# Kernel tuning notes

Measured on AMD Instinct MI355X. Metric: run time of the kernel, lower is better.

Reference implementation:

```python
import jax, jax.numpy as jnp
import numpy as np
from jax import lax

DT = 0.1


def setup_inputs() -> dict:
    key = jax.random.key(0)
    k1, k2, k3, k4 = jax.random.split(key, 4)
    Bsz, L, D, N, O = 32, 2048, 256, 64, 256
    x = jax.random.normal(k1, (Bsz, L, D), dtype=jnp.float32)
    # Shift A by 3*I so Re(eig(A)) > 0 -> bilinear-discretized A_tilde is stable
    A = jax.random.uniform(k2, (N, N), dtype=jnp.float32) + 3.0 * jnp.eye(N, dtype=jnp.float32)
    B = jax.random.uniform(k3, (N, D), dtype=jnp.float32)
    C = jax.random.uniform(k4, (O, N), dtype=jnp.float32)
    return {"x": x, "A": A, "B": B, "C": C}


def _s4_forward(x, A, B, C):
    N = A.shape[0]
    I = jnp.eye(N, dtype=A.dtype)
    # Bilinear discretization (as written in the torch source)
    tmp_inv = jnp.linalg.inv(I + A * (DT / 2))
    A_tilde = tmp_inv @ (I - A * (DT / 2))          # [N, N]
    B_tilde = (tmp_inv @ B) * DT                    # [N, D]

    L = x.shape[1]

    # K[i] = C @ A_tilde^i @ B_tilde; carry M = A_tilde^i @ B_tilde
    def step(M, _):
        return A_tilde @ M, C @ M                    # emit [O, D]

    _, K = lax.scan(step, B_tilde, None, length=L)   # K: [L, O, D]

    n = 2 * L - 1  # length after torch's F.pad(x, (0,0,0,L-1))
    x_fft = jnp.fft.rfft(x, n=n, axis=1)             # [B, F, D] complex
    K_fft = jnp.fft.rfft(K, n=n, axis=0)             # [F, O, D] complex
    y_fft = jnp.einsum('bfi,foi->bfo', x_fft, K_fft)
    y = jnp.fft.irfft(y_fft, n=n, axis=1)[:, :L]     # [B, L, O]
    return y


def reference(x, A, B, C):
    return _s4_forward(x, A, B, C)
```

## Files before the change

### kernel.cpp

```cpp
#include <hip/hip_runtime.h>

#define B_SZ   32
#define LEN    2048
#define DIM    256
#define NST    64
#define OUTD   256
#define CHUNK  64
#define NCHUNK (LEN / CHUNK)
#define ROWS   (B_SZ * LEN)

#define OFF_AT   0
#define OFF_A64  4096
#define OFF_MT   8192
#define OFF_S    12288
#define OFF_INST 77824
#define OFF_U    143360
#define OFF_H    4337664
#define OFF_V    OFF_H
#define WS_FLOATS (OFF_H + ROWS * 64)

__global__ __launch_bounds__(256) void k_fused0(const float* __restrict__ A,
                                                const float* __restrict__ Bm,
                                                const float* __restrict__ x,
                                                float* __restrict__ ws) {
  __shared__ __align__(16) float sh[9088];
  const int t = threadIdx.x;

  if (blockIdx.x == 0) {
    float* Pa  = sh;
    float* Pb  = sh + 4352;
    float* rbM = sh + 8704;
    float* rbI = sh + 8832;
    float* cb  = sh + 8960;

    const int tc = t & 63;
    const int tr = t >> 6;
    float M[16], Iv[16];
    for (int i = 0; i < 16; ++i) {
      int r = 16 * tr + i;
      M[i] = 0.05f * A[r * 64 + tc] + (r == tc ? 1.0f : 0.0f);
      Iv[i] = (r == tc) ? 1.0f : 0.0f;
    }
    if (tr == 0) { rbM[tc] = M[0]; rbI[tc] = Iv[0]; }
    if (tc == 0)
      for (int i = 0; i < 16; ++i) cb[16 * tr + i] = M[i];
    __syncthreads();

#pragma unroll
    for (int k = 0; k < 64; ++k) {
      const int cur = (k & 1) * 64, nxt = ((k + 1) & 1) * 64;
      float rinv = 1.0f / rbM[cur + k];
      float rM = rbM[cur + tc] * rinv;
      float rI = rbI[cur + tc] * rinv;
#pragma unroll
      for (int i = 0; i < 16; ++i) {
        int r = 16 * tr + i;
        if (r == k) { M[i] = rM; Iv[i] = rI; }
        else {
          float f = cb[cur + r];
          M[i] = fmaf(-f, rM, M[i]);
          Iv[i] = fmaf(-f, rI, Iv[i]);
        }
      }
      if (k < 63) {
        if (tr == ((k + 1) >> 4)) {
          rbM[nxt + tc] = M[(k + 1) & 15];
          rbI[nxt + tc] = Iv[(k + 1) & 15];
        }
        if (tc == k + 1)
          for (int i = 0; i < 16; ++i) cb[nxt + 16 * tr + i] = M[i];
      }
      __syncthreads();
    }

    for (int i = 0; i < 16; ++i) {
      int r = 16 * tr + i;
      ws[OFF_AT + r * 64 + tc] = 2.0f * Iv[i] - (r == tc ? 1.0f : 0.0f);
      Pa[r * 65 + tc] = Iv[i];
    }
    __syncthreads();
    for (int i = 0; i < 16; ++i) {
      int m = 16 * tr + i;
      ws[OFF_MT + m * 64 + tc] = Pa[tc * 65 + m];
    }
    __syncthreads();

    for (int i = 0; i < 16; ++i) {
      int r = 16 * tr + i;
      Pa[r * 68 + tc] = 2.0f * Iv[i] - (r == tc ? 1.0f : 0.0f);
    }
    __syncthreads();
    float* src = Pa; float* dst = Pb;
    const int r0 = 4 * (t >> 4), c0 = 4 * (t & 15);
    for (int it = 0; it < 6; ++it) {
      float acc[4][4] = {};
      for (int k = 0; k < 64; ++k) {
        float4 bv = *(const float4*)(src + k * 68 + c0);
        for (int i = 0; i < 4; ++i) {
          float av = src[(r0 + i) * 68 + k];
          acc[i][0] = fmaf(av, bv.x, acc[i][0]);
          acc[i][1] = fmaf(av, bv.y, acc[i][1]);
          acc[i][2] = fmaf(av, bv.z, acc[i][2]);
          acc[i][3] = fmaf(av, bv.w, acc[i][3]);
        }
      }
      for (int i = 0; i < 4; ++i)
        *(float4*)(dst + (r0 + i) * 68 + c0) =
            make_float4(acc[i][0], acc[i][1], acc[i][2], acc[i][3]);
      __syncthreads();
      float* tmp = src; src = dst; dst = tmp;
    }
    for (int i = 0; i < 4; ++i) {
      int f = 4 * (t + 256 * i);
      int r = f >> 6, c = f & 63;
      *(float4*)(ws + OFF_A64 + f) = *(const float4*)(src + r * 68 + c);
    }
  } else {
    float* xsT = sh;
    float* bsT = sh + 4352;
    const int rowbase = (blockIdx.x - 1) * 64;
    const int r0 = 4 * (t >> 4), m0 = 4 * (t & 15);
    float acc[4][4] = {};
    for (int db = 0; db < 4; ++db) {
      int d0 = db * 64;
      for (int i = 0; i < 4; ++i) {
        int e = 4 * (t + 256 * i);
        int rr = e >> 6, dd = e & 63;
        float4 xv = *(const float4*)(x + (size_t)(rowbase + rr) * 256 + d0 + dd);
        xsT[(dd + 0) * 68 + rr] = xv.x;
        xsT[(dd + 1) * 68 + rr] = xv.y;
        xsT[(dd + 2) * 68 + rr] = xv.z;
        xsT[(dd + 3) * 68 + rr] = xv.w;
        float4 bv = *(const float4*)(Bm + (size_t)rr * 256 + d0 + dd);
        bsT[(dd + 0) * 68 + rr] = bv.x;
        bsT[(dd + 1) * 68 + rr] = bv.y;
        bsT[(dd + 2) * 68 + rr] = bv.z;
        bsT[(dd + 3) * 68 + rr] = bv.w;
      }
      __syncthreads();
      for (int k = 0; k < 64; ++k) {
        float4 av4 = *(const float4*)(xsT + k * 68 + r0);
        float4 bv4 = *(const float4*)(bsT + k * 68 + m0);
        float av[4] = {av4.x, av4.y, av4.z, av4.w};
        float bv[4] = {bv4.x, bv4.y, bv4.z, bv4.w};
        for (int i = 0; i < 4; ++i)
          for (int j = 0; j < 4; ++j) acc[i][j] = fmaf(av[i], bv[j], acc[i][j]);
      }
      __syncthreads();
    }
    float* v = ws + OFF_V;
    for (int i = 0; i < 4; ++i)
      *(float4*)(v + (size_t)(rowbase + r0 + i) * 64 + m0) =
          make_float4(acc[i][0], acc[i][1], acc[i][2], acc[i][3]);
  }
}

__global__ __launch_bounds__(256) void k_umm(float* __restrict__ ws) {
  __shared__ __align__(16) float vT[64 * 68];
  __shared__ __align__(16) float mts[64 * 68];
  const int t = threadIdx.x;
  const int rowbase = blockIdx.x * 64;
  const float* v = ws + OFF_V;
  for (int i = 0; i < 4; ++i) {
    int e = 4 * (t + 256 * i);
    int rr = e >> 6, mm = e & 63;
    *(float4*)(mts + rr * 68 + mm) = *(const float4*)(ws + OFF_MT + e);
    float4 vv = *(const float4*)(v + (size_t)(rowbase + rr) * 64 + mm);
    vT[(mm + 0) * 68 + rr] = vv.x;
    vT[(mm + 1) * 68 + rr] = vv.y;
    vT[(mm + 2) * 68 + rr] = vv.z;
    vT[(mm + 3) * 68 + rr] = vv.w;
  }
  __syncthreads();
  const int r0 = 4 * (t >> 4), n0 = 4 * (t & 15);
  float acc[4][4] = {};
  for (int k = 0; k < 64; ++k) {
    float4 av4 = *(const float4*)(vT + k * 68 + r0);
    float4 bv4 = *(const float4*)(mts + k * 68 + n0);
    float av[4] = {av4.x, av4.y, av4.z, av4.w};
    float bv[4] = {bv4.x, bv4.y, bv4.z, bv4.w};
    for (int i = 0; i < 4; ++i)
      for (int j = 0; j < 4; ++j) acc[i][j] = fmaf(av[i], bv[j], acc[i][j]);
  }
  float* u = ws + OFF_U;
  for (int i = 0; i < 4; ++i)
    *(float4*)(u + (size_t)(rowbase + r0 + i) * 64 + n0) =
        make_float4(0.1f * acc[i][0], 0.1f * acc[i][1], 0.1f * acc[i][2],
                    0.1f * acc[i][3]);
}

__device__ __forceinline__ void load_areg(const float* __restrict__ M, int r,
                                          int q, float areg[16]) {
  const float4* ap = (const float4*)(M + r * 64 + q * 16);
  float4 a0 = ap[0], a1 = ap[1], a2 = ap[2], a3 = ap[3];
  areg[0] = a0.x; areg[1] = a0.y; areg[2] = a0.z; areg[3] = a0.w;
  areg[4] = a1.x; areg[5] = a1.y; areg[6] = a1.z; areg[7] = a1.w;
  areg[8] = a2.x; areg[9] = a2.y; areg[10] = a2.z; areg[11] = a2.w;
  areg[12] = a3.x; areg[13] = a3.y; areg[14] = a3.z; areg[15] = a3.w;
}

__device__ __forceinline__ float matvec_step(const float areg[16],
                                             const float* __restrict__ hcur,
                                             float* __restrict__ part, int r,
                                             int q, int t) {
  float4 ha = *(const float4*)(hcur + q * 16);
  float4 hb = *(const float4*)(hcur + q * 16 + 4);
  float4 hc = *(const float4*)(hcur + q * 16 + 8);
  float4 hd = *(const float4*)(hcur + q * 16 + 12);
  float p0 = fmaf(areg[0], ha.x, fmaf(areg[4], hb.x, fmaf(areg[8], hc.x, areg[12] * hd.x)));
  float p1 = fmaf(areg[1], ha.y, fmaf(areg[5], hb.y, fmaf(areg[9], hc.y, areg[13] * hd.y)));
  float p2 = fmaf(areg[2], ha.z, fmaf(areg[6], hb.z, fmaf(areg[10], hc.z, areg[14] * hd.z)));
  float p3 = fmaf(areg[3], ha.w, fmaf(areg[7], hb.w, fmaf(areg[11], hc.w, areg[15] * hd.w)));
  part[q * 68 + r] = (p0 + p1) + (p2 + p3);
  __syncthreads();
  float s = 0.0f;
  if (t < 64) s = part[t] + part[68 + t] + part[136 + t] + part[204 + t];
  return s;
}

__global__ __launch_bounds__(256) void k_chunk(float* __restrict__ ws, int phase) {
  __shared__ __align__(16) float hcur[64];
  __shared__ __align__(16) float part[4 * 68];
  __shared__ __align__(16) float ulds[CHUNK * 64];
  const int t = threadIdx.x;
  const int c = blockIdx.x, b = blockIdx.y;
  const int r = t & 63, q = t >> 6;
  float areg[16];
  load_areg(ws + OFF_AT, r, q, areg);
  const float* u = ws + OFF_U + (size_t)(b * LEN + c * CHUNK) * 64;
  for (int i = 0; i < 4; ++i) {
    int e = 4 * (t + 256 * i);
    *(float4*)(ulds + e) = *(const float4*)(u + e);
  }
  if (t < 64)
    hcur[t] = (phase == 3) ? ws[OFF_INST + (b * NCHUNK + c) * 64 + t] : 0.0f;
  __syncthreads();
  for (int st = 0; st < CHUNK; ++st) {
    float s = matvec_step(areg, hcur, part, r, q, t);
    if (t < 64) {
      float hn = s + ulds[st * 64 + t];
      hcur[t] = hn;
      if (phase == 3)
        ws[OFF_H + (size_t)(b * LEN + c * CHUNK + st) * 64 + t] = hn;
      else if (st == CHUNK - 1)
        ws[OFF_S + (b * NCHUNK + c) * 64 + t] = hn;
    }
    __syncthreads();
  }
}

__global__ __launch_bounds__(256) void k_carry(float* __restrict__ ws) {
  __shared__ __align__(16) float hcur[64];
  __shared__ __align__(16) float part[4 * 68];
  __shared__ __align__(16) float slds[NCHUNK * 64];
  const int t = threadIdx.x;
  const int b = blockIdx.x;
  const int r = t & 63, q = t >> 6;
  float areg[16];
  load_areg(ws + OFF_A64, r, q, areg);
  for (int i = 0; i < 2; ++i) {
    int e = 4 * (t + 256 * i);
    *(float4*)(slds + e) = *(const float4*)(ws + OFF_S + b * NCHUNK * 64 + e);
  }
  if (t < 64) {
    hcur[t] = 0.0f;
    ws[OFF_INST + (b * NCHUNK) * 64 + t] = 0.0f;
  }
  __syncthreads();
  for (int c = 1; c < NCHUNK; ++c) {
    float s = matvec_step(areg, hcur, part, r, q, t);
    if (t < 64) {
      float hn = s + slds[(c - 1) * 64 + t];
      hcur[t] = hn;
      ws[OFF_INST + (b * NCHUNK + c) * 64 + t] = hn;
    }
    __syncthreads();
  }
}

__global__ __launch_bounds__(256) void k_ygemm(const float* __restrict__ Cm,
                                               const float* __restrict__ ws,
                                               float* __restrict__ y) {
  __shared__ __align__(16) float hs[64 * 68];
  __shared__ __align__(16) float cs[64 * 68];
  const int t = threadIdx.x;
  const int rowbase = blockIdx.x * 64;
  const int o0 = blockIdx.y * 64;
  const float* h = ws + OFF_H;
  for (int i = 0; i < 4; ++i) {
    int e = 4 * (t + 256 * i);
    int rr = e >> 6, nn = e & 63;
    *(float4*)(hs + rr * 68 + nn) =
        *(const float4*)(h + (size_t)rowbase * 64 + e);
    float4 cv = *(const float4*)(Cm + (size_t)(o0 + rr) * 64 + nn);
    cs[(nn + 0) * 68 + rr] = cv.x;
    cs[(nn + 1) * 68 + rr] = cv.y;
    cs[(nn + 2) * 68 + rr] = cv.z;
    cs[(nn + 3) * 68 + rr] = cv.w;
  }
  __syncthreads();
  const int tr = t >> 4, tc = t & 15;
  const int r0 = tr * 4, c0 = tc * 4;
  float acc[4][4] = {};
  for (int k = 0; k < 64; ++k) {
    float4 cv4 = *(const float4*)(cs + k * 68 + c0);
    float cv[4] = {cv4.x, cv4.y, cv4.z, cv4.w};
    for (int i = 0; i < 4; ++i) {
      float hv = hs[(r0 + i) * 68 + k];
      for (int j = 0; j < 4; ++j) acc[i][j] = fmaf(hv, cv[j], acc[i][j]);
    }
  }
  for (int i = 0; i < 4; ++i)
    *(float4*)(y + (size_t)(rowbase + r0 + i) * 256 + o0 + c0) =
        make_float4(acc[i][0], acc[i][1], acc[i][2], acc[i][3]);
}

extern "C" void kernel_launch(void* const* d_in, const int* in_sizes, int n_in,
                              void* d_out, int out_size, void* d_ws,
                              size_t ws_size, hipStream_t stream) {
  const float* x = (const float*)d_in[0];
  const float* A = (const float*)d_in[1];
  const float* Bm = (const float*)d_in[2];
  const float* Cm = (const float*)d_in[3];
  float* y = (float*)d_out;
  float* ws = (float*)d_ws;
  if (ws_size < (size_t)WS_FLOATS * sizeof(float)) return;

  hipLaunchKernelGGL(k_fused0, dim3(1 + ROWS / 64), dim3(256), 0, stream, A, Bm,
                     x, ws);
  hipLaunchKernelGGL(k_umm, dim3(ROWS / 64), dim3(256), 0, stream, ws);
  hipLaunchKernelGGL(k_chunk, dim3(NCHUNK, B_SZ), dim3(256), 0, stream, ws, 1);
  hipLaunchKernelGGL(k_carry, dim3(B_SZ), dim3(256), 0, stream, ws);
  hipLaunchKernelGGL(k_chunk, dim3(NCHUNK, B_SZ), dim3(256), 0, stream, ws, 3);
  hipLaunchKernelGGL(k_ygemm, dim3(ROWS / 64, OUTD / 64), dim3(256), 0, stream,
                     Cm, ws, y);
}
```

Measured before the change: 259.6 us.

## Precompute Btilde/C^T in one prep block, use wave-level readlane matvec scan

A single prep block now computes the scaled B_tilde (inverse times B times DT) and a transposed copy of C. This folds the two-step x->v->u projection into one GEMM, k_ugemm, reading x directly. The chunk scan and the carry kernel now run one wave per chunk, holding a full A row in 64 registers and broadcasting h with readlane. That drops the LDS partial sums and the block barriers from each step. k_ygemm loops over all four output tiles per block and reads pre-transposed C, so the carry kernel writes the incoming states in place of a separate buffer. In exchange, the serial prep block on one CU grows, and the 64-register A rows raise register pressure.

```diff
diff --git a/kernel.cpp b/kernel.cpp
--- a/kernel.cpp
+++ b/kernel.cpp
@@ -11,85 +11,107 @@
 
 #define OFF_AT   0
 #define OFF_A64  4096
-#define OFF_MT   8192
-#define OFF_S    12288
-#define OFF_INST 77824
-#define OFF_U    143360
-#define OFF_H    4337664
-#define OFF_V    OFF_H
+#define OFF_BT   8192
+#define OFF_CT   24576
+#define OFF_S    40960
+#define OFF_U    106496
+#define OFF_H    4300800
 #define WS_FLOATS (OFF_H + ROWS * 64)
 
-__global__ __launch_bounds__(256) void k_fused0(const float* __restrict__ A,
-                                                const float* __restrict__ Bm,
-                                                const float* __restrict__ x,
-                                                float* __restrict__ ws) {
-  __shared__ __align__(16) float sh[9088];
-  const int t = threadIdx.x;
-
-  if (blockIdx.x == 0) {
-    float* Pa  = sh;
-    float* Pb  = sh + 4352;
-    float* rbM = sh + 8704;
-    float* rbI = sh + 8832;
-    float* cb  = sh + 8960;
-
-    const int tc = t & 63;
-    const int tr = t >> 6;
-    float M[16], Iv[16];
+__global__ __launch_bounds__(256) void k_prep(const float* __restrict__ A,
+                                              const float* __restrict__ Bm,
+                                              const float* __restrict__ Cm,
+                                              float* __restrict__ ws) {
+  __shared__ __align__(16) float sh[13440];
+  float* Ilds = sh;
+  float* Pa   = sh + 4352;
+  float* Pb   = sh + 8704;
+  float* rbM  = sh + 13056;
+  float* rbI  = sh + 13184;
+  float* cb   = sh + 13312;
+  float* bs   = Pa;
+  float* cs   = Pa;
+
+  const int t  = threadIdx.x;
+  const int tc = t & 63;
+  const int tr = t >> 6;
+
+  float M[16], Iv[16];
+  for (int i = 0; i < 16; ++i) {
+    int r = 16 * tr + i;
+    M[i] = 0.05f * A[r * 64 + tc] + (r == tc ? 1.0f : 0.0f);
+    Iv[i] = (r == tc) ? 1.0f : 0.0f;
+  }
+  if (tr == 0) { rbM[tc] = M[0]; rbI[tc] = Iv[0]; }
+  if (tc == 0)
+    for (int i = 0; i < 16; ++i) cb[16 * tr + i] = M[i];
+  __syncthreads();
+
+#pragma unroll
+  for (int k = 0; k < 64; ++k) {
+    const int cur = (k & 1) * 64, nxt = ((k + 1) & 1) * 64;
+    float rinv = 1.0f / rbM[cur + k];
+    float rM = rbM[cur + tc] * rinv;
+    float rI = rbI[cur + tc] * rinv;
+#pragma unroll
     for (int i = 0; i < 16; ++i) {
       int r = 16 * tr + i;
-      M[i] = 0.05f * A[r * 64 + tc] + (r == tc ? 1.0f : 0.0f);
-      Iv[i] = (r == tc) ? 1.0f : 0.0f;
-    }
-    if (tr == 0) { rbM[tc] = M[0]; rbI[tc] = Iv[0]; }
-    if (tc == 0)
-      for (int i = 0; i < 16; ++i) cb[16 * tr + i] = M[i];
-    __syncthreads();
-
-#pragma unroll
-    for (int k = 0; k < 64; ++k) {
-      const int cur = (k & 1) * 64, nxt = ((k + 1) & 1) * 64;
-      float rinv = 1.0f / rbM[cur + k];
-      float rM = rbM[cur + tc] * rinv;
-      float rI = rbI[cur + tc] * rinv;
-#pragma unroll
-      for (int i = 0; i < 16; ++i) {
-        int r = 16 * tr + i;
-        if (r == k) { M[i] = rM; Iv[i] = rI; }
-        else {
-          float f = cb[cur + r];
-          M[i] = fmaf(-f, rM, M[i]);
-          Iv[i] = fmaf(-f, rI, Iv[i]);
-        }
-      }
-      if (k < 63) {
-        if (tr == ((k + 1) >> 4)) {
-          rbM[nxt + tc] = M[(k + 1) & 15];
-          rbI[nxt + tc] = Iv[(k + 1) & 15];
-        }
-        if (tc == k + 1)
-          for (int i = 0; i < 16; ++i) cb[nxt + 16 * tr + i] = M[i];
+      if (r == k) { M[i] = rM; Iv[i] = rI; }
+      else {
+        float f = cb[cur + r];
+        M[i] = fmaf(-f, rM, M[i]);
+        Iv[i] = fmaf(-f, rI, Iv[i]);
+      }
+    }
+    if (k < 63) {
+      if (tr == ((k + 1) >> 4)) {
+        rbM[nxt + tc] = M[(k + 1) & 15];
+        rbI[nxt + tc] = Iv[(k + 1) & 15];
+      }
+      if (tc == k + 1)
+        for (int i = 0; i < 16; ++i) cb[nxt + 16 * tr + i] = M[i];
+    }
+    __syncthreads();
+  }
+
+  for (int i = 0; i < 16; ++i) {
+    int r = 16 * tr + i;
+    ws[OFF_AT + r * 64 + tc] = 2.0f * Iv[i] - (r == tc ? 1.0f : 0.0f);
+    Ilds[r * 65 + tc] = Iv[i];
+  }
+  __syncthreads();
+
+  {
+    const int n = tc, g = tr;
+    for (int rd = 0; rd < 4; ++rd) {
+      int d0 = rd * 64;
+      for (int i = 0; i < 4; ++i) {
+        int e = 4 * (t + 256 * i);
+        int kk = e >> 6, dd = e & 63;
+        *(float4*)(bs + kk * 68 + dd) =
+            *(const float4*)(Bm + kk * 256 + d0 + dd);
       }
       __syncthreads();
-    }
-
-    for (int i = 0; i < 16; ++i) {
-      int r = 16 * tr + i;
-      ws[OFF_AT + r * 64 + tc] = 2.0f * Iv[i] - (r == tc ? 1.0f : 0.0f);
-      Pa[r * 65 + tc] = Iv[i];
-    }
-    __syncthreads();
-    for (int i = 0; i < 16; ++i) {
-      int m = 16 * tr + i;
-      ws[OFF_MT + m * 64 + tc] = Pa[tc * 65 + m];
-    }
-    __syncthreads();
-
-    for (int i = 0; i < 16; ++i) {
-      int r = 16 * tr + i;
-      Pa[r * 68 + tc] = 2.0f * Iv[i] - (r == tc ? 1.0f : 0.0f);
-    }
-    __syncthreads();
+      float acc[16] = {};
+      for (int k = 0; k < 64; ++k) {
+        float av = Ilds[n * 65 + k];
+#pragma unroll
+        for (int j = 0; j < 16; ++j)
+          acc[j] = fmaf(av, bs[k * 68 + g * 16 + j], acc[j]);
+      }
+      for (int j = 0; j < 16; ++j)
+        ws[OFF_BT + (d0 + g * 16 + j) * 64 + n] = 0.1f * acc[j];
+      __syncthreads();
+    }
+  }
+
+  for (int i = 0; i < 16; ++i) {
+    int idx = t + 256 * i;
+    int r = idx >> 6, c = idx & 63;
+    Pa[r * 68 + c] = 2.0f * Ilds[r * 65 + c] - (r == c ? 1.0f : 0.0f);
+  }
+  __syncthreads();
+  {
     float* src = Pa; float* dst = Pb;
     const int r0 = 4 * (t >> 4), c0 = 4 * (t & 15);
     for (int it = 0; it < 6; ++it) {
@@ -115,204 +137,161 @@
       int r = f >> 6, c = f & 63;
       *(float4*)(ws + OFF_A64 + f) = *(const float4*)(src + r * 68 + c);
     }
-  } else {
-    float* xsT = sh;
-    float* bsT = sh + 4352;
-    const int rowbase = (blockIdx.x - 1) * 64;
-    const int r0 = 4 * (t >> 4), m0 = 4 * (t & 15);
-    float acc[4][4] = {};
-    for (int db = 0; db < 4; ++db) {
-      int d0 = db * 64;
-      for (int i = 0; i < 4; ++i) {
-        int e = 4 * (t + 256 * i);
-        int rr = e >> 6, dd = e & 63;
-        float4 xv = *(const float4*)(x + (size_t)(rowbase + rr) * 256 + d0 + dd);
-        xsT[(dd + 0) * 68 + rr] = xv.x;
-        xsT[(dd + 1) * 68 + rr] = xv.y;
-        xsT[(dd + 2) * 68 + rr] = xv.z;
-        xsT[(dd + 3) * 68 + rr] = xv.w;
-        float4 bv = *(const float4*)(Bm + (size_t)rr * 256 + d0 + dd);
-        bsT[(dd + 0) * 68 + rr] = bv.x;
-        bsT[(dd + 1) * 68 + rr] = bv.y;
-        bsT[(dd + 2) * 68 + rr] = bv.z;
-        bsT[(dd + 3) * 68 + rr] = bv.w;
-      }
-      __syncthreads();
-      for (int k = 0; k < 64; ++k) {
-        float4 av4 = *(const float4*)(xsT + k * 68 + r0);
-        float4 bv4 = *(const float4*)(bsT + k * 68 + m0);
-        float av[4] = {av4.x, av4.y, av4.z, av4.w};
-        float bv[4] = {bv4.x, bv4.y, bv4.z, bv4.w};
-        for (int i = 0; i < 4; ++i)
-          for (int j = 0; j < 4; ++j) acc[i][j] = fmaf(av[i], bv[j], acc[i][j]);
-      }
-      __syncthreads();
-    }
-    float* v = ws + OFF_V;
-    for (int i = 0; i < 4; ++i)
-      *(float4*)(v + (size_t)(rowbase + r0 + i) * 64 + m0) =
-          make_float4(acc[i][0], acc[i][1], acc[i][2], acc[i][3]);
-  }
-}
-
-__global__ __launch_bounds__(256) void k_umm(float* __restrict__ ws) {
-  __shared__ __align__(16) float vT[64 * 68];
-  __shared__ __align__(16) float mts[64 * 68];
+  }
+  __syncthreads();
+
+  for (int ob = 0; ob < 4; ++ob) {
+    int o0 = ob * 64;
+    for (int i = 0; i < 16; ++i) {
+      int idx = t + 256 * i;
+      int oo = idx >> 6, nn = idx & 63;
+      cs[oo * 65 + nn] = Cm[(size_t)(o0 + oo) * 64 + nn];
+    }
+    __syncthreads();
+    for (int i = 0; i < 16; ++i) {
+      int idx = t + 256 * i;
+      int nn = idx >> 6, oo = idx & 63;
+      ws[OFF_CT + nn * 256 + o0 + oo] = cs[oo * 65 + nn];
+    }
+    __syncthreads();
+  }
+}
+
+__global__ __launch_bounds__(256) void k_ugemm(const float* __restrict__ x,
+                                               float* __restrict__ ws) {
+  __shared__ __align__(16) float xs[64 * 68];
+  __shared__ __align__(16) float bs[64 * 68];
+  const float* Bt = ws + OFF_BT;
+  float* u = ws + OFF_U;
   const int t = threadIdx.x;
   const int rowbase = blockIdx.x * 64;
-  const float* v = ws + OFF_V;
-  for (int i = 0; i < 4; ++i) {
-    int e = 4 * (t + 256 * i);
-    int rr = e >> 6, mm = e & 63;
-    *(float4*)(mts + rr * 68 + mm) = *(const float4*)(ws + OFF_MT + e);
-    float4 vv = *(const float4*)(v + (size_t)(rowbase + rr) * 64 + mm);
-    vT[(mm + 0) * 68 + rr] = vv.x;
-    vT[(mm + 1) * 68 + rr] = vv.y;
-    vT[(mm + 2) * 68 + rr] = vv.z;
-    vT[(mm + 3) * 68 + rr] = vv.w;
-  }
-  __syncthreads();
   const int r0 = 4 * (t >> 4), n0 = 4 * (t & 15);
   float acc[4][4] = {};
-  for (int k = 0; k < 64; ++k) {
-    float4 av4 = *(const float4*)(vT + k * 68 + r0);
-    float4 bv4 = *(const float4*)(mts + k * 68 + n0);
-    float av[4] = {av4.x, av4.y, av4.z, av4.w};
-    float bv[4] = {bv4.x, bv4.y, bv4.z, bv4.w};
-    for (int i = 0; i < 4; ++i)
-      for (int j = 0; j < 4; ++j) acc[i][j] = fmaf(av[i], bv[j], acc[i][j]);
-  }
-  float* u = ws + OFF_U;
+  for (int db = 0; db < 4; ++db) {
+    int d0 = db * 64;
+    for (int i = 0; i < 4; ++i) {
+      int e = 4 * (t + 256 * i);
+      int rr = e >> 6, dd = e & 63;
+      *(float4*)(xs + rr * 68 + dd) =
+          *(const float4*)(x + (size_t)(rowbase + rr) * 256 + d0 + dd);
+      *(float4*)(bs + rr * 68 + dd) = *(const float4*)(Bt + d0 * 64 + e);
+    }
+    __syncthreads();
+    for (int k = 0; k < 64; ++k) {
+      float4 bv4 = *(const float4*)(bs + k * 68 + n0);
+      for (int i = 0; i < 4; ++i) {
+        float av = xs[(r0 + i) * 68 + k];
+        acc[i][0] = fmaf(av, bv4.x, acc[i][0]);
+        acc[i][1] = fmaf(av, bv4.y, acc[i][1]);
+        acc[i][2] = fmaf(av, bv4.z, acc[i][2]);
+        acc[i][3] = fmaf(av, bv4.w, acc[i][3]);
+      }
+    }
+    __syncthreads();
+  }
   for (int i = 0; i < 4; ++i)
     *(float4*)(u + (size_t)(rowbase + r0 + i) * 64 + n0) =
-        make_float4(0.1f * acc[i][0], 0.1f * acc[i][1], 0.1f * acc[i][2],
-                    0.1f * acc[i][3]);
-}
-
-__device__ __forceinline__ void load_areg(const float* __restrict__ M, int r,
-                                          int q, float areg[16]) {
-  const float4* ap = (const float4*)(M + r * 64 + q * 16);
-  float4 a0 = ap[0], a1 = ap[1], a2 = ap[2], a3 = ap[3];
-  areg[0] = a0.x; areg[1] = a0.y; areg[2] = a0.z; areg[3] = a0.w;
-  areg[4] = a1.x; areg[5] = a1.y; areg[6] = a1.z; areg[7] = a1.w;
-  areg[8] = a2.x; areg[9] = a2.y; areg[10] = a2.z; areg[11] = a2.w;
-  areg[12] = a3.x; areg[13] = a3.y; areg[14] = a3.z; areg[15] = a3.w;
-}
-
-__device__ __forceinline__ float matvec_step(const float areg[16],
-                                             const float* __restrict__ hcur,
-                                             float* __restrict__ part, int r,
-                                             int q, int t) {
-  float4 ha = *(const float4*)(hcur + q * 16);
-  float4 hb = *(const float4*)(hcur + q * 16 + 4);
-  float4 hc = *(const float4*)(hcur + q * 16 + 8);
-  float4 hd = *(const float4*)(hcur + q * 16 + 12);
-  float p0 = fmaf(areg[0], ha.x, fmaf(areg[4], hb.x, fmaf(areg[8], hc.x, areg[12] * hd.x)));
-  float p1 = fmaf(areg[1], ha.y, fmaf(areg[5], hb.y, fmaf(areg[9], hc.y, areg[13] * hd.y)));
-  float p2 = fmaf(areg[2], ha.z, fmaf(areg[6], hb.z, fmaf(areg[10], hc.z, areg[14] * hd.z)));
-  float p3 = fmaf(areg[3], ha.w, fmaf(areg[7], hb.w, fmaf(areg[11], hc.w, areg[15] * hd.w)));
-  part[q * 68 + r] = (p0 + p1) + (p2 + p3);
-  __syncthreads();
-  float s = 0.0f;
-  if (t < 64) s = part[t] + part[68 + t] + part[136 + t] + part[204 + t];
-  return s;
+        make_float4(acc[i][0], acc[i][1], acc[i][2], acc[i][3]);
+}
+
+__device__ __forceinline__ float bcast(float v, int lane) {
+  return __int_as_float(__builtin_amdgcn_readlane(__float_as_int(v), lane));
+}
+
+__device__ __forceinline__ float wave_matvec(const float areg[64], float h) {
+  float a0 = 0.f, a1 = 0.f, a2 = 0.f, a3 = 0.f;
+#pragma unroll
+  for (int m = 0; m < 16; ++m) {
+    a0 = fmaf(areg[m], bcast(h, m), a0);
+    a1 = fmaf(areg[m + 16], bcast(h, m + 16), a1);
+    a2 = fmaf(areg[m + 32], bcast(h, m + 32), a2);
+    a3 = fmaf(areg[m + 48], bcast(h, m + 48), a3);
+  }
+  return (a0 + a1) + (a2 + a3);
+}
+
+__device__ __forceinline__ void load_arow(const float* __restrict__ M, int r,
+                                          float areg[64]) {
+#pragma unroll
+  for (int i = 0; i < 16; ++i)
+    *(float4*)(areg + 4 * i) = *(const float4*)(M + r * 64 + 4 * i);
 }
 
 __global__ __launch_bounds__(256) void k_chunk(float* __restrict__ ws, int phase) {
-  __shared__ __align__(16) float hcur[64];
-  __shared__ __align__(16) float part[4 * 68];
-  __shared__ __align__(16) float ulds[CHUNK * 64];
   const int t = threadIdx.x;
-  const int c = blockIdx.x, b = blockIdx.y;
-  const int r = t & 63, q = t >> 6;
-  float areg[16];
-  load_areg(ws + OFF_AT, r, q, areg);
-  const float* u = ws + OFF_U + (size_t)(b * LEN + c * CHUNK) * 64;
-  for (int i = 0; i < 4; ++i) {
-    int e = 4 * (t + 256 * i);
-    *(float4*)(ulds + e) = *(const float4*)(u + e);
-  }
-  if (t < 64)
-    hcur[t] = (phase == 3) ? ws[OFF_INST + (b * NCHUNK + c) * 64 + t] : 0.0f;
-  __syncthreads();
+  const int r = t & 63, wid = t >> 6;
+  const int c = blockIdx.x * 4 + wid, b = blockIdx.y;
+  float areg[64];
+  load_arow(ws + OFF_AT, r, areg);
+  const float* uptr = ws + OFF_U + (size_t)(b * LEN + c * CHUNK) * 64;
+  float* Hout = ws + OFF_H + (size_t)(b * LEN + c * CHUNK) * 64;
+  float h = 0.f;
+  if (phase == 2 && c > 0) h = ws[OFF_S + (b * NCHUNK + c - 1) * 64 + r];
+  float ucur = uptr[r];
+#pragma unroll 1
   for (int st = 0; st < CHUNK; ++st) {
-    float s = matvec_step(areg, hcur, part, r, q, t);
-    if (t < 64) {
-      float hn = s + ulds[st * 64 + t];
-      hcur[t] = hn;
-      if (phase == 3)
-        ws[OFF_H + (size_t)(b * LEN + c * CHUNK + st) * 64 + t] = hn;
-      else if (st == CHUNK - 1)
-        ws[OFF_S + (b * NCHUNK + c) * 64 + t] = hn;
-    }
-    __syncthreads();
-  }
-}
-
-__global__ __launch_bounds__(256) void k_carry(float* __restrict__ ws) {
-  __shared__ __align__(16) float hcur[64];
-  __shared__ __align__(16) float part[4 * 68];
-  __shared__ __align__(16) float slds[NCHUNK * 64];
-  const int t = threadIdx.x;
+    float unxt = (st + 1 < CHUNK) ? uptr[(st + 1) * 64 + r] : 0.f;
+    h = wave_matvec(areg, h) + ucur;
+    if (phase == 2) Hout[st * 64 + r] = h;
+    ucur = unxt;
+  }
+  if (phase == 1) ws[OFF_S + (b * NCHUNK + c) * 64 + r] = h;
+}
+
+__global__ __launch_bounds__(64) void k_carry(float* __restrict__ ws) {
+  const int r = threadIdx.x;
   const int b = blockIdx.x;
-  const int r = t & 63, q = t >> 6;
-  float areg[16];
-  load_areg(ws + OFF_A64, r, q, areg);
-  for (int i = 0; i < 2; ++i) {
-    int e = 4 * (t + 256 * i);
-    *(float4*)(slds + e) = *(const float4*)(ws + OFF_S + b * NCHUNK * 64 + e);
-  }
-  if (t < 64) {
-    hcur[t] = 0.0f;
-    ws[OFF_INST + (b * NCHUNK) * 64 + t] = 0.0f;
-  }
-  __syncthreads();
+  float areg[64];
+  load_arow(ws + OFF_A64, r, areg);
+  float* S = ws + OFF_S + b * NCHUNK * 64;
+  float h = 0.f;
+#pragma unroll 1
   for (int c = 1; c < NCHUNK; ++c) {
-    float s = matvec_step(areg, hcur, part, r, q, t);
-    if (t < 64) {
-      float hn = s + slds[(c - 1) * 64 + t];
-      hcur[t] = hn;
-      ws[OFF_INST + (b * NCHUNK + c) * 64 + t] = hn;
-    }
-    __syncthreads();
-  }
-}
-
-__global__ __launch_bounds__(256) void k_ygemm(const float* __restrict__ Cm,
-                                               const float* __restrict__ ws,
+    float sv = S[(c - 1) * 64 + r];
+    h = wave_matvec(areg, h) + sv;
+    S[(c - 1) * 64 + r] = h;
+  }
+}
+
+__global__ __launch_bounds__(256) void k_ygemm(float* __restrict__ ws,
                                                float* __restrict__ y) {
   __shared__ __align__(16) float hs[64 * 68];
-  __shared__ __align__(16) float cs[64 * 68];
+  __shared__ __align__(16) float ct[64 * 68];
   const int t = threadIdx.x;
   const int rowbase = blockIdx.x * 64;
-  const int o0 = blockIdx.y * 64;
-  const float* h = ws + OFF_H;
+  const float* H = ws + OFF_H;
+  const float* CT = ws + OFF_CT;
   for (int i = 0; i < 4; ++i) {
     int e = 4 * (t + 256 * i);
     int rr = e >> 6, nn = e & 63;
     *(float4*)(hs + rr * 68 + nn) =
-        *(const float4*)(h + (size_t)rowbase * 64 + e);
-    float4 cv = *(const float4*)(Cm + (size_t)(o0 + rr) * 64 + nn);
-    cs[(nn + 0) * 68 + rr] = cv.x;
-    cs[(nn + 1) * 68 + rr] = cv.y;
-    cs[(nn + 2) * 68 + rr] = cv.z;
-    cs[(nn + 3) * 68 + rr] = cv.w;
-  }
-  __syncthreads();
-  const int tr = t >> 4, tc = t & 15;
-  const int r0 = tr * 4, c0 = tc * 4;
-  float acc[4][4] = {};
-  for (int k = 0; k < 64; ++k) {
-    float4 cv4 = *(const float4*)(cs + k * 68 + c0);
-    float cv[4] = {cv4.x, cv4.y, cv4.z, cv4.w};
+        *(const float4*)(H + (size_t)rowbase * 64 + e);
+  }
+  const int r0 = 4 * (t >> 4), c0 = 4 * (t & 15);
+  for (int ob = 0; ob < 4; ++ob) {
+    int o0 = ob * 64;
+    __syncthreads();
     for (int i = 0; i < 4; ++i) {
-      float hv = hs[(r0 + i) * 68 + k];
-      for (int j = 0; j < 4; ++j) acc[i][j] = fmaf(hv, cv[j], acc[i][j]);
-    }
-  }
-  for (int i = 0; i < 4; ++i)
-    *(float4*)(y + (size_t)(rowbase + r0 + i) * 256 + o0 + c0) =
-        make_float4(acc[i][0], acc[i][1], acc[i][2], acc[i][3]);
+      int e = 4 * (t + 256 * i);
+      int nn = e >> 6, oo = e & 63;
+      *(float4*)(ct + nn * 68 + oo) = *(const float4*)(CT + nn * 256 + o0 + oo);
+    }
+    __syncthreads();
+    float acc[4][4] = {};
+    for (int k = 0; k < 64; ++k) {
+      float4 cv4 = *(const float4*)(ct + k * 68 + c0);
+      for (int i = 0; i < 4; ++i) {
+        float hv = hs[(r0 + i) * 68 + k];
+        acc[i][0] = fmaf(hv, cv4.x, acc[i][0]);
+        acc[i][1] = fmaf(hv, cv4.y, acc[i][1]);
+        acc[i][2] = fmaf(hv, cv4.z, acc[i][2]);
+        acc[i][3] = fmaf(hv, cv4.w, acc[i][3]);
+      }
+    }
+    for (int i = 0; i < 4; ++i)
+      *(float4*)(y + (size_t)(rowbase + r0 + i) * 256 + o0 + c0) =
+          make_float4(acc[i][0], acc[i][1], acc[i][2], acc[i][3]);
+  }
 }
 
 extern "C" void kernel_launch(void* const* d_in, const int* in_sizes, int n_in,
@@ -326,12 +305,10 @@
   float* ws = (float*)d_ws;
   if (ws_size < (size_t)WS_FLOATS * sizeof(float)) return;
 
-  hipLaunchKernelGGL(k_fused0, dim3(1 + ROWS / 64), dim3(256), 0, stream, A, Bm,
-                     x, ws);
-  hipLaunchKernelGGL(k_umm, dim3(ROWS / 64), dim3(256), 0, stream, ws);
-  hipLaunchKernelGGL(k_chunk, dim3(NCHUNK, B_SZ), dim3(256), 0, stream, ws, 1);
-  hipLaunchKernelGGL(k_carry, dim3(B_SZ), dim3(256), 0, stream, ws);
-  hipLaunchKernelGGL(k_chunk, dim3(NCHUNK, B_SZ), dim3(256), 0, stream, ws, 3);
-  hipLaunchKernelGGL(k_ygemm, dim3(ROWS / 64, OUTD / 64), dim3(256), 0, stream,
-                     Cm, ws, y);
-}
+  hipLaunchKernelGGL(k_prep, dim3(1), dim3(256), 0, stream, A, Bm, Cm, ws);
+  hipLaunchKernelGGL(k_ugemm, dim3(ROWS / 64), dim3(256), 0, stream, x, ws);
+  hipLaunchKernelGGL(k_chunk, dim3(NCHUNK / 4, B_SZ), dim3(256), 0, stream, ws, 1);
+  hipLaunchKernelGGL(k_carry, dim3(B_SZ), dim3(64), 0, stream, ws);
+  hipLaunchKernelGGL(k_chunk, dim3(NCHUNK / 4, B_SZ), dim3(256), 0, stream, ws, 2);
+  hipLaunchKernelGGL(k_ygemm, dim3(ROWS / 64), dim3(256), 0, stream, ws, y);
+}
```

New measurement: 317.1 us. +22.1%, slower.
